# Kernel optimization log

Measured on AMD Instinct MI355X. Metric: run time of the kernel, lower is better.

Reference implementation:

```python
import jax, jax.numpy as jnp
import numpy as np

BATCH, IN, OUT, G = 2048, 512, 512, 8


def setup_inputs() -> dict:
    key = jax.random.key(0)
    k1, k2, k3 = jax.random.split(key, 3)
    x = jax.random.normal(k1, (BATCH, IN), dtype=jnp.float32)
    # spline coefficients, initialized small like normal_(c, 0, 0.001)
    c = jax.random.normal(k2, (G, OUT, IN), dtype=jnp.float32) * 0.001
    # residual weights, xavier-like small init
    w_b = jax.random.normal(k3, (OUT, IN), dtype=jnp.float32) * 0.001
    w_s = jnp.ones((OUT, IN), dtype=jnp.float32)
    # RBF grid centers over [-2, 2] (get_size() == G)
    grid = jnp.arange(G, dtype=jnp.float32) * (4.0 / (G - 1)) - 2.0
    return {"x": x, "c": c, "w_b": w_b, "w_s": w_s, "grid": grid}


def _basis(x, grid):
    # Gaussian RBF basis: [batch, G, in]
    d = x[:, None, :] - grid[None, :, None]
    return jnp.exp(-(d * d))


def reference(x, c, w_b, w_s, grid):
    basis_vals = _basis(x, grid)                      # [b, n=G, i]
    # faithful to th.einsum('bni,aoi->boi', ...): n and a are independently summed
    spline_out = jnp.einsum('bni,aoi->boi', basis_vals, c)  # [b, o, i]
    spline_out = spline_out * w_s[None]
    res_out = jax.nn.silu(x)[:, None, :] * w_b[None]  # [b, o, i]
    return (spline_out + res_out).sum(axis=-1)        # [b, o]
```

## Files before the change

kernel.cpp:

```cpp
#include <hip/hip_runtime.h>

#define BATCH 2048
#define IN    512
#define OUT   512
#define NG    8
#define KTOT  1024

#define TILE_SHORTS 4096
#define NIT 16

typedef __attribute__((ext_vector_type(8))) short bf16x8;
typedef __attribute__((ext_vector_type(4))) float f32x4;

__device__ inline unsigned short f2bf(float f) {
    union { float f; unsigned int u; } v; v.f = f;
    unsigned int r = v.u + 0x7fffu + ((v.u >> 16) & 1u);
    return (unsigned short)(r >> 16);
}

__device__ inline void gload_lds16(const void* g, void* l) {
    __builtin_amdgcn_global_load_lds((const __attribute__((address_space(1))) void*)g,
                                     (__attribute__((address_space(3))) void*)l, 16, 0, 0);
}

__global__ __launch_bounds__(256) void prep_kernel(const float* __restrict__ x,
                                                   const float* __restrict__ c,
                                                   const float* __restrict__ w_b,
                                                   const float* __restrict__ w_s,
                                                   const float* __restrict__ grid,
                                                   unsigned short* __restrict__ A,
                                                   unsigned short* __restrict__ B) {
    int blk = blockIdx.x;
    int tid = threadIdx.x;
    int lane6 = tid & 63;
    int kt = lane6 >> 3;
    int cc = lane6 & 7;
    if (blk < 512) {
        int b   = blk * 4 + (tid >> 6);
        int e   = b * IN + lane6 * 8;
        int mt  = b >> 6, row = b & 63;
        int swc = cc ^ (row & 7);
        float g0 = grid[0];
        float dl = grid[1] - g0;
        float d2 = dl * dl;
        float dn[NG];
#pragma unroll
        for (int n = 0; n < NG; ++n) dn[n] = __expf(-d2 * (float)(n * n));
        float4 x0 = *(const float4*)&x[e];
        float4 x1 = *(const float4*)&x[e + 4];
        float xv[8] = {x0.x, x0.y, x0.z, x0.w, x1.x, x1.y, x1.z, x1.w};
        unsigned short sv[8], lv[8];
#pragma unroll
        for (int j = 0; j < 8; ++j) {
            float u  = xv[j] - g0;
            float e1 = __expf(-u * u);
            float q  = __expf(2.f * dl * u);
            float p  = dn[NG - 1];
#pragma unroll
            for (int n = NG - 2; n >= 0; --n) p = p * q + dn[n];
            sv[j] = f2bf(e1 * p);
            lv[j] = f2bf(xv[j] / (1.f + __expf(-xv[j])));
        }
        *(int4*)&A[(mt * 16 + kt)     * TILE_SHORTS + row * 64 + swc * 8] = *(int4*)sv;
        *(int4*)&A[(mt * 16 + 8 + kt) * TILE_SHORTS + row * 64 + swc * 8] = *(int4*)lv;
    } else {
        int o   = (blk - 512) * 4 + (tid >> 6);
        int e   = o * IN + lane6 * 8;
        int nt  = o >> 6, row = o & 63;
        int swc = cc ^ (row & 7);
        float acc[8] = {};
#pragma unroll
        for (int a = 0; a < NG; ++a) {
            float4 c0 = *(const float4*)&c[(size_t)a * (OUT * IN) + e];
            float4 c1 = *(const float4*)&c[(size_t)a * (OUT * IN) + e + 4];
            acc[0] += c0.x; acc[1] += c0.y; acc[2] += c0.z; acc[3] += c0.w;
            acc[4] += c1.x; acc[5] += c1.y; acc[6] += c1.z; acc[7] += c1.w;
        }
        float4 s0 = *(const float4*)&w_s[e];
        float4 s1 = *(const float4*)&w_s[e + 4];
        float sw[8] = {s0.x, s0.y, s0.z, s0.w, s1.x, s1.y, s1.z, s1.w};
        float4 b0 = *(const float4*)&w_b[e];
        float4 b1 = *(const float4*)&w_b[e + 4];
        float bw[8] = {b0.x, b0.y, b0.z, b0.w, b1.x, b1.y, b1.z, b1.w};
        unsigned short cv[8], bv[8];
#pragma unroll
        for (int j = 0; j < 8; ++j) { cv[j] = f2bf(acc[j] * sw[j]); bv[j] = f2bf(bw[j]); }
        *(int4*)&B[(nt * 16 + kt)     * TILE_SHORTS + row * 64 + swc * 8] = *(int4*)cv;
        *(int4*)&B[(nt * 16 + 8 + kt) * TILE_SHORTS + row * 64 + swc * 8] = *(int4*)bv;
    }
}

__global__ __launch_bounds__(512) void gemm_kernel(const unsigned short* __restrict__ A,
                                                   const unsigned short* __restrict__ B,
                                                   float* __restrict__ outp) {
    __shared__ short As[2][TILE_SHORTS];
    __shared__ short Bs[2][TILE_SHORTS];

    int tid  = threadIdx.x;
    int lane = tid & 63;
    int w    = tid >> 6;
    int wm   = (w >> 2) & 1;
    int wn   = (w >> 1) & 1;
    int ks   = w & 1;
    int lr   = lane & 15, lg = lane >> 4;

    int bid  = blockIdx.x;
    int mg   = bid & 7;
    int rest = bid >> 3;
    int sub  = rest >> 3;
    int ncol = rest & 7;
    int mt   = mg * 4 + sub;
    int m0   = mt * 64;
    int n0   = ncol * 64;

    const unsigned short* Ab = A + (size_t)(mt * 16) * TILE_SHORTS;
    const unsigned short* Bb = B + (size_t)(ncol * 16) * TILE_SHORTS;

    int swc  = ((ks * 4 + lg) ^ (lr & 7)) * 8;
    int ra0  = (wm * 32 + lr)      * 64 + swc;
    int ra1  = (wm * 32 + 16 + lr) * 64 + swc;
    int rb0  = (wn * 32 + lr)      * 64 + swc;
    int rb1  = (wn * 32 + 16 + lr) * 64 + swc;

    f32x4 acc00 = {0.f, 0.f, 0.f, 0.f};
    f32x4 acc01 = {0.f, 0.f, 0.f, 0.f};
    f32x4 acc10 = {0.f, 0.f, 0.f, 0.f};
    f32x4 acc11 = {0.f, 0.f, 0.f, 0.f};

    gload_lds16(Ab + tid * 8, &As[0][tid * 8]);
    gload_lds16(Bb + tid * 8, &Bs[0][tid * 8]);
    __syncthreads();

#pragma unroll
    for (int it = 0; it < NIT; ++it) {
        int cur = it & 1;
        if (it + 1 < NIT) {
            gload_lds16(Ab + (it + 1) * TILE_SHORTS + tid * 8, &As[cur ^ 1][tid * 8]);
            gload_lds16(Bb + (it + 1) * TILE_SHORTS + tid * 8, &Bs[cur ^ 1][tid * 8]);
        }
        bf16x8 a0 = *(const bf16x8*)&As[cur][ra0];
        bf16x8 a1 = *(const bf16x8*)&As[cur][ra1];
        bf16x8 b0 = *(const bf16x8*)&Bs[cur][rb0];
        bf16x8 b1 = *(const bf16x8*)&Bs[cur][rb1];
        acc00 = __builtin_amdgcn_mfma_f32_16x16x32_bf16(a0, b0, acc00, 0, 0, 0);
        acc01 = __builtin_amdgcn_mfma_f32_16x16x32_bf16(a0, b1, acc01, 0, 0, 0);
        acc10 = __builtin_amdgcn_mfma_f32_16x16x32_bf16(a1, b0, acc10, 0, 0, 0);
        acc11 = __builtin_amdgcn_mfma_f32_16x16x32_bf16(a1, b1, acc11, 0, 0, 0);
        __syncthreads();
    }

    float* Ls = (float*)&As[0][0];
    int p = w >> 1;
    if (ks == 1) {
        *(f32x4*)&Ls[p * 1024 + lane * 16 + 0]  = acc00;
        *(f32x4*)&Ls[p * 1024 + lane * 16 + 4]  = acc01;
        *(f32x4*)&Ls[p * 1024 + lane * 16 + 8]  = acc10;
        *(f32x4*)&Ls[p * 1024 + lane * 16 + 12] = acc11;
    }
    __syncthreads();
    if (ks == 0) {
        f32x4 p00 = *(const f32x4*)&Ls[p * 1024 + lane * 16 + 0];
        f32x4 p01 = *(const f32x4*)&Ls[p * 1024 + lane * 16 + 4];
        f32x4 p10 = *(const f32x4*)&Ls[p * 1024 + lane * 16 + 8];
        f32x4 p11 = *(const f32x4*)&Ls[p * 1024 + lane * 16 + 12];
        int orow = m0 + wm * 32 + lg * 4;
        int ocol = n0 + wn * 32 + lr;
#pragma unroll
        for (int r = 0; r < 4; ++r) {
            outp[(size_t)(orow + r) * OUT + ocol]           = acc00[r] + p00[r];
            outp[(size_t)(orow + r) * OUT + ocol + 16]      = acc01[r] + p01[r];
            outp[(size_t)(orow + 16 + r) * OUT + ocol]      = acc10[r] + p10[r];
            outp[(size_t)(orow + 16 + r) * OUT + ocol + 16] = acc11[r] + p11[r];
        }
    }
}

extern "C" void kernel_launch(void* const* d_in, const int* in_sizes, int n_in,
                              void* d_out, int out_size, void* d_ws, size_t ws_size,
                              hipStream_t stream) {
    (void)in_sizes; (void)n_in; (void)out_size; (void)ws_size;
    const float* x    = (const float*)d_in[0];
    const float* c    = (const float*)d_in[1];
    const float* w_b  = (const float*)d_in[2];
    const float* w_s  = (const float*)d_in[3];
    const float* grid = (const float*)d_in[4];
    float* outp = (float*)d_out;

    unsigned short* A = (unsigned short*)d_ws;
    unsigned short* B = A + (size_t)BATCH * KTOT;

    prep_kernel<<<512 + 128, 256, 0, stream>>>(x, c, w_b, w_s, grid, A, B);
    gemm_kernel<<<256, 512, 0, stream>>>(A, B, outp);
}
```

Measured before the change: 21.06 us.

## Triple-buffer GEMM LDS loads with vmcnt waits and use row-major prep layout

```diff
diff --git a/kernel.cpp b/kernel.cpp
--- a/kernel.cpp
+++ b/kernel.cpp
@@ -32,14 +32,8 @@
                                                    unsigned short* __restrict__ B) {
     int blk = blockIdx.x;
     int tid = threadIdx.x;
-    int lane6 = tid & 63;
-    int kt = lane6 >> 3;
-    int cc = lane6 & 7;
     if (blk < 512) {
-        int b   = blk * 4 + (tid >> 6);
-        int e   = b * IN + lane6 * 8;
-        int mt  = b >> 6, row = b & 63;
-        int swc = cc ^ (row & 7);
+        int e = (blk * 256 + tid) * 8;
         float g0 = grid[0];
         float dl = grid[1] - g0;
         float d2 = dl * dl;
@@ -61,13 +55,11 @@
             sv[j] = f2bf(e1 * p);
             lv[j] = f2bf(xv[j] / (1.f + __expf(-xv[j])));
         }
-        *(int4*)&A[(mt * 16 + kt)     * TILE_SHORTS + row * 64 + swc * 8] = *(int4*)sv;
-        *(int4*)&A[(mt * 16 + 8 + kt) * TILE_SHORTS + row * 64 + swc * 8] = *(int4*)lv;
+        int b = e >> 9, i = e & 511;
+        *(int4*)&A[b * KTOT + i]       = *(int4*)sv;
+        *(int4*)&A[b * KTOT + 512 + i] = *(int4*)lv;
     } else {
-        int o   = (blk - 512) * 4 + (tid >> 6);
-        int e   = o * IN + lane6 * 8;
-        int nt  = o >> 6, row = o & 63;
-        int swc = cc ^ (row & 7);
+        int e = ((blk - 512) * 256 + tid) * 8;
         float acc[8] = {};
 #pragma unroll
         for (int a = 0; a < NG; ++a) {
@@ -85,16 +77,17 @@
         unsigned short cv[8], bv[8];
 #pragma unroll
         for (int j = 0; j < 8; ++j) { cv[j] = f2bf(acc[j] * sw[j]); bv[j] = f2bf(bw[j]); }
-        *(int4*)&B[(nt * 16 + kt)     * TILE_SHORTS + row * 64 + swc * 8] = *(int4*)cv;
-        *(int4*)&B[(nt * 16 + 8 + kt) * TILE_SHORTS + row * 64 + swc * 8] = *(int4*)bv;
+        int o = e >> 9, i = e & 511;
+        *(int4*)&B[o * KTOT + i]       = *(int4*)cv;
+        *(int4*)&B[o * KTOT + 512 + i] = *(int4*)bv;
     }
 }
 
 __global__ __launch_bounds__(512) void gemm_kernel(const unsigned short* __restrict__ A,
                                                    const unsigned short* __restrict__ B,
                                                    float* __restrict__ outp) {
-    __shared__ short As[2][TILE_SHORTS];
-    __shared__ short Bs[2][TILE_SHORTS];
+    __shared__ short As[3][TILE_SHORTS];
+    __shared__ short Bs[3][TILE_SHORTS];
 
     int tid  = threadIdx.x;
     int lane = tid & 63;
@@ -113,8 +106,10 @@
     int m0   = mt * 64;
     int n0   = ncol * 64;
 
-    const unsigned short* Ab = A + (size_t)(mt * 16) * TILE_SHORTS;
-    const unsigned short* Bb = B + (size_t)(ncol * 16) * TILE_SHORTS;
+    int srow = tid >> 3;
+    int gsc  = (tid & 7) ^ (srow & 7);
+    const unsigned short* a_src = A + (size_t)(m0 + srow) * KTOT + gsc * 8;
+    const unsigned short* b_src = B + (size_t)(n0 + srow) * KTOT + gsc * 8;
 
     int swc  = ((ks * 4 + lg) ^ (lr & 7)) * 8;
     int ra0  = (wm * 32 + lr)      * 64 + swc;
@@ -127,17 +122,21 @@
     f32x4 acc10 = {0.f, 0.f, 0.f, 0.f};
     f32x4 acc11 = {0.f, 0.f, 0.f, 0.f};
 
-    gload_lds16(Ab + tid * 8, &As[0][tid * 8]);
-    gload_lds16(Bb + tid * 8, &Bs[0][tid * 8]);
-    __syncthreads();
+#define STAGE(t, buf) do { \
+        gload_lds16(a_src + (t) * 64, &As[buf][tid * 8]); \
+        gload_lds16(b_src + (t) * 64, &Bs[buf][tid * 8]); \
+    } while (0)
+
+    STAGE(0, 0);
+    STAGE(1, 1);
+    asm volatile("s_waitcnt vmcnt(2)" ::: "memory");
+    __builtin_amdgcn_s_barrier();
+    __builtin_amdgcn_sched_barrier(0);
 
 #pragma unroll
     for (int it = 0; it < NIT; ++it) {
-        int cur = it & 1;
-        if (it + 1 < NIT) {
-            gload_lds16(Ab + (it + 1) * TILE_SHORTS + tid * 8, &As[cur ^ 1][tid * 8]);
-            gload_lds16(Bb + (it + 1) * TILE_SHORTS + tid * 8, &Bs[cur ^ 1][tid * 8]);
-        }
+        int cur = it % 3;
+        if (it + 2 < NIT) STAGE(it + 2, (it + 2) % 3);
         bf16x8 a0 = *(const bf16x8*)&As[cur][ra0];
         bf16x8 a1 = *(const bf16x8*)&As[cur][ra1];
         bf16x8 b0 = *(const bf16x8*)&Bs[cur][rb0];
@@ -146,9 +145,16 @@
         acc01 = __builtin_amdgcn_mfma_f32_16x16x32_bf16(a0, b1, acc01, 0, 0, 0);
         acc10 = __builtin_amdgcn_mfma_f32_16x16x32_bf16(a1, b0, acc10, 0, 0, 0);
         acc11 = __builtin_amdgcn_mfma_f32_16x16x32_bf16(a1, b1, acc11, 0, 0, 0);
-        __syncthreads();
-    }
-
+        if (it + 1 < NIT) {
+            if (it + 2 < NIT) asm volatile("s_waitcnt vmcnt(2)" ::: "memory");
+            else              asm volatile("s_waitcnt vmcnt(0)" ::: "memory");
+            __builtin_amdgcn_s_barrier();
+            __builtin_amdgcn_sched_barrier(0);
+        }
+    }
+#undef STAGE
+
+    __syncthreads();
     float* Ls = (float*)&As[0][0];
     int p = w >> 1;
     if (ks == 1) {
```

After: 18.40 us. 12.6% less time.
